# Kernel optimization log

Hardware: AMD Instinct MI355X
Metric: run time of the kernel (lower is better)

## Reference

```python
import jax, jax.numpy as jnp
import numpy as np

M0, M1, H = 128, 64, 8            # scalar mul, vector mul, num heads
AH0, AH1 = 16, 8                  # per-head irreps: 16x0e + 8x1e
D = M0 + 3 * M1                   # 320 node feature dim
DTP0 = M0 + M1                    # 192 scalar channels out of depthwise TP
DTP1 = M0 + 2 * M1                # 256 vector channels out of depthwise TP
WNUM = 2 * M0 + 3 * M1            # 448 TP path weights (uvu, edge mul=1)
RAD_IN, RAD_HID = 32, 64
N_NODES, N_EDGES = 10000, 160000
INV_SQRT3 = 1.0 / np.sqrt(3.0)    # CG norm for 1e x 1e -> 0e
INV_SQRT2 = 1.0 / np.sqrt(2.0)    # CG norm for 1e x 1e -> 1e


def _split(x, m0, m1):
    # e3nn layout: [m0 scalars | m1 vectors * 3 components]
    return x[..., :m0], x[..., m0:].reshape(x.shape[:-1] + (m1, 3))


def _silu(x):
    return x * jax.nn.sigmoid(x)


def _smooth_leaky(x, a=0.2):
    # SmoothLeakyReLU from equiformer
    return 0.5 * (1 + a) * x + 0.5 * (1 - a) * x * (2.0 * jax.nn.sigmoid(x) - 1.0)


def _dtp(s, v, e0, e1, w):
    # depthwise (uvu) tensor product of (M0x0e + M1x1e) with edge attr (1x0e + 1x1e)
    # s [E,M0], v [E,M1,3], e0 [E,1], e1 [E,3], w [E,WNUM] or [WNUM] (internal)
    w1, w2, w3, w4, w5 = jnp.split(w, [M0, 2 * M0, 2 * M0 + M1, 2 * M0 + 2 * M1], axis=-1)
    os1 = w1 * s * e0                                                  # 0e x 0e -> 0e
    os2 = w4 * (jnp.einsum('emc,ec->em', v, e1) * INV_SQRT3)           # 1e x 1e -> 0e
    ov1 = (w2 * s)[..., None] * e1[:, None, :]                         # 0e x 1e -> 1e
    ov2 = w3[..., None] * v * e0[..., None]                            # 1e x 0e -> 1e
    ov3 = w5[..., None] * (jnp.cross(v, e1[:, None, :]) * INV_SQRT2)   # 1e x 1e -> 1e
    return jnp.concatenate([os1, os2], -1), jnp.concatenate([ov1, ov2, ov3], -2)


def _forward(node_input, edge_src, edge_dst, edge_attr, edge_scalars,
             Wsrc_s, Wsrc_v, bsrc, Wdst_s, Wdst_v,
             rad_W1, rad_b1, rad_W2, rad_off,
             Wact_s, bact, Wact_v, Walpha, balpha, w_int,
             Wval_s, bval, Wval_v, alpha_dot, Wproj_s, bproj, Wproj_v):
    N = node_input.shape[0]
    E = edge_src.shape[0]
    s, v = _split(node_input, M0, M1)
    # merge_src / merge_dst: per-irrep linear (bias only on scalars of src)
    ms_s = s @ Wsrc_s + bsrc
    ms_v = jnp.einsum('nmc,mk->nkc', v, Wsrc_v)
    md_s = s @ Wdst_s
    md_v = jnp.einsum('nmc,mk->nkc', v, Wdst_v)
    msg_s = ms_s[edge_src] + md_s[edge_dst]          # [E, M0]
    msg_v = ms_v[edge_src] + md_v[edge_dst]          # [E, M1, 3]
    e0, e1 = edge_attr[:, :1], edge_attr[:, 1:4]
    # radial profile MLP -> edge-dependent TP weights
    w = _silu(edge_scalars @ rad_W1 + rad_b1) @ rad_W2 + rad_off       # [E, WNUM]
    ds, dv = _dtp(msg_s, msg_v, e0, e1, w)           # [E, DTP0], [E, DTP1, 3]
    # alpha branch: linear on TP scalars -> heads -> smooth leaky -> dot
    al = _smooth_leaky((ds @ Walpha + balpha).reshape(E, H, AH0))
    logits = jnp.einsum('ehk,hk->eh', al, alpha_dot[0])                # [E, H]
    # value branch: sep_act.lin + gate
    scal = ds @ Wact_s + bact                        # [E, M0+M1] scalars+gates
    gated_v = jnp.einsum('emc,mk->ekc', dv, Wact_v)  # [E, M1, 3]
    val_s = _silu(scal[:, :M0])
    val_v = gated_v * jax.nn.sigmoid(scal[:, M0:])[..., None]
    # sep_value: depthwise TP with internal weights + linear
    vs, vv = _dtp(val_s, val_v, e0, e1, w_int)
    out_s = vs @ Wval_s + bval                       # [E, H*AH0]
    out_v = jnp.einsum('emc,mk->ekc', vv, Wval_v)    # [E, H*AH1, 3]
    value = jnp.concatenate([out_s.reshape(E, H, AH0),
                             out_v.reshape(E, H, AH1 * 3)], axis=2)    # [E, H, 40]
    # softmax over incoming edges per destination node
    mx = jax.lax.stop_gradient(jax.ops.segment_max(logits, edge_dst, num_segments=N))
    mx = jnp.where(jnp.isfinite(mx), mx, 0.0)
    ex = jnp.exp(logits - mx[edge_dst])
    den = jax.ops.segment_sum(ex, edge_dst, num_segments=N)
    alpha = ex / (den[edge_dst] + 1e-16)             # [E, H]
    agg = jax.ops.segment_sum(value * alpha[..., None], edge_dst, num_segments=N)
    # heads2vec + output projection
    node_s = agg[:, :, :AH0].reshape(N, H * AH0)
    node_v = agg[:, :, AH0:].reshape(N, H * AH1, 3)
    po_s = node_s @ Wproj_s + bproj
    po_v = jnp.einsum('nmc,mk->nkc', node_v, Wproj_v)
    return jnp.concatenate([po_s, po_v.reshape(N, M1 * 3)], axis=1)


def _lin(key, fi, fo):
    return jax.random.normal(key, (fi, fo), jnp.float32) / np.sqrt(fi)


def setup_inputs() -> dict:
    ks = iter(jax.random.split(jax.random.key(0), 40))
    inp = {}
    inp['node_input'] = jax.random.normal(next(ks), (N_NODES, D), jnp.float32)
    inp['edge_src'] = jax.random.randint(next(ks), (N_EDGES,), 0, N_NODES)
    inp['edge_dst'] = jax.random.randint(next(ks), (N_EDGES,), 0, N_NODES)
    inp['edge_attr'] = jax.random.normal(next(ks), (N_EDGES, 4), jnp.float32)
    inp['edge_scalars'] = jax.random.normal(next(ks), (N_EDGES, RAD_IN), jnp.float32)
    inp['Wsrc_s'] = _lin(next(ks), M0, M0)
    inp['Wsrc_v'] = _lin(next(ks), M1, M1)
    inp['bsrc'] = 0.1 * jax.random.normal(next(ks), (M0,), jnp.float32)
    inp['Wdst_s'] = _lin(next(ks), M0, M0)
    inp['Wdst_v'] = _lin(next(ks), M1, M1)
    inp['rad_W1'] = _lin(next(ks), RAD_IN, RAD_HID)
    inp['rad_b1'] = 0.1 * jax.random.normal(next(ks), (RAD_HID,), jnp.float32)
    inp['rad_W2'] = _lin(next(ks), RAD_HID, WNUM)
    inp['rad_off'] = 0.1 * jax.random.normal(next(ks), (WNUM,), jnp.float32)
    inp['Wact_s'] = _lin(next(ks), DTP0, M0 + M1)
    inp['bact'] = 0.1 * jax.random.normal(next(ks), (M0 + M1,), jnp.float32)
    inp['Wact_v'] = _lin(next(ks), DTP1, M1)
    inp['Walpha'] = _lin(next(ks), DTP0, H * AH0)
    inp['balpha'] = 0.1 * jax.random.normal(next(ks), (H * AH0,), jnp.float32)
    inp['w_int'] = jax.random.normal(next(ks), (WNUM,), jnp.float32)
    inp['Wval_s'] = _lin(next(ks), DTP0, H * AH0)
    inp['bval'] = 0.1 * jax.random.normal(next(ks), (H * AH0,), jnp.float32)
    inp['Wval_v'] = _lin(next(ks), DTP1, H * AH1)
    inp['alpha_dot'] = jax.random.normal(next(ks), (1, H, AH0), jnp.float32) / np.sqrt(AH0)
    inp['Wproj_s'] = _lin(next(ks), H * AH0, M0)
    inp['bproj'] = 0.1 * jax.random.normal(next(ks), (M0,), jnp.float32)
    inp['Wproj_v'] = _lin(next(ks), H * AH1, M1)
    return inp


def reference(node_input, edge_src, edge_dst, edge_attr, edge_scalars,
              Wsrc_s, Wsrc_v, bsrc, Wdst_s, Wdst_v,
              rad_W1, rad_b1, rad_W2, rad_off,
              Wact_s, bact, Wact_v, Walpha, balpha, w_int,
              Wval_s, bval, Wval_v, alpha_dot, Wproj_s, bproj, Wproj_v):
    return _forward(node_input, edge_src, edge_dst, edge_attr, edge_scalars,
                    Wsrc_s, Wsrc_v, bsrc, Wdst_s, Wdst_v,
                    rad_W1, rad_b1, rad_W2, rad_off,
                    Wact_s, bact, Wact_v, Walpha, balpha, w_int,
                    Wval_s, bval, Wval_v, alpha_dot, Wproj_s, bproj, Wproj_v)
```

## Files before the change

### kernel.cpp

```cpp
#include <hip/hip_runtime.h>

#define NN 10000
#define NE 160000
#define INV_SQRT3f 0.57735026918962576f
#define INV_SQRT2f 0.70710678118654752f
#define VPLU 640000

typedef short bshort8 __attribute__((ext_vector_type(8)));
typedef float floatx4 __attribute__((ext_vector_type(4)));
#define MFMA16(a,b,c) __builtin_amdgcn_mfma_f32_16x16x32_bf16((a),(b),(c),0,0,0)

__device__ __forceinline__ float sigm(float x){ return 1.f/(1.f+__expf(-x)); }
__device__ __forceinline__ float siluf(float x){ return x*sigm(x); }
__device__ __forceinline__ float sleaky(float x){ return 0.6f*x + 0.4f*x*(2.f*sigm(x)-1.f); }
__device__ __forceinline__ unsigned short f2bf(float f){
  return (unsigned short)((__float_as_uint(f) + 0x8000u)>>16);
}
__device__ __forceinline__ float bf2f(unsigned short h){
  return __uint_as_float(((unsigned)h)<<16);
}
__device__ __forceinline__ unsigned cvtpk(float lo, float hi){
  unsigned r;
  asm("v_cvt_pk_bf16_f32 %0, %1, %2" : "=v"(r) : "v"(lo), "v"(hi));
  return r;
}

#define O_W1   0
#define O_W2   2048
#define O_WAS  30720
#define O_WAVT 67584
#define O_WAVB 75776
#define O_WVS  83968
#define O_WVVT 108544
#define O_WVVB 116736
#define O_WALP 124928
#define SWZ_TOTAL 149504

__global__ __launch_bounds__(256) void k_pre_all(
    const float* __restrict__ x,
    const float* __restrict__ Wsrc_s, const float* __restrict__ Wsrc_v,
    const float* __restrict__ bsrc,
    const float* __restrict__ Wdst_s, const float* __restrict__ Wdst_v,
    unsigned short* __restrict__ ms_s, unsigned short* __restrict__ md_s,
    unsigned short* __restrict__ ms_v, unsigned short* __restrict__ md_v,
    const float* __restrict__ W1, const float* __restrict__ W2,
    const float* __restrict__ WAs, const float* __restrict__ WAv,
    const float* __restrict__ WVs, const float* __restrict__ WVv,
    const float* __restrict__ WAl, const float* __restrict__ w_int,
    unsigned short* __restrict__ swz,
    float* __restrict__ num, float* __restrict__ den, int* __restrict__ cnt) {
  __shared__ __align__(16) float s_s[128*8];
  __shared__ __align__(16) float s_v[192*8];
  const int tid = threadIdx.x;
  const int b = blockIdx.x;
  if (b >= 1834) {
    int base = (b-1834)*256 + tid;
    float4 z = {0.f,0.f,0.f,0.f};
    for (int i = base; i < 800000; i += 554496) ((float4*)num)[i] = z;
    if (base < 20000) ((float4*)den)[base] = z;
    if (base < 10000) cnt[base] = 0;
    return;
  }
  if (b >= 1250) {
    int s = (b-1250)*256 + tid;
    if (s >= SWZ_TOTAL) return;
    const float* src; int base, N, KT, rowOff;
    if      (s < 2048)  { base=O_W1;   src=W1;  N=64;  KT=1; rowOff=0; }
    else if (s < 30720) { base=O_W2;   src=W2;  N=448; KT=2; rowOff=0; }
    else if (s < 67584) { base=O_WAS;  src=WAs; N=192; KT=6; rowOff=0; }
    else if (s < 75776) { base=O_WAVT; src=WAv; N=64;  KT=4; rowOff=0; }
    else if (s < 83968) { base=O_WAVB; src=WAv; N=64;  KT=4; rowOff=128; }
    else if (s < 108544){ base=O_WVS;  src=WVs; N=128; KT=6; rowOff=0; }
    else if (s < 116736){ base=O_WVVT; src=WVv; N=64;  KT=4; rowOff=0; }
    else if (s < 124928){ base=O_WVVB; src=WVv; N=64;  KT=4; rowOff=128; }
    else                { base=O_WALP; src=WAl; N=128; KT=6; rowOff=0; }
    int loc = s - base;
    int j = loc & 7, l = (loc>>3)&63, kt = (loc>>9)%KT, nt = loc/(512*KT);
    int row = kt*32 + (l>>4)*8 + j + rowOff;
    int col = nt*16 + (l&15);
    float scl = 1.f;
    if      (base == O_WVS)  scl = (row < 128) ? w_int[row] : w_int[192+row]*INV_SQRT3f;
    else if (base == O_WVVT) scl = w_int[128+row];
    else if (base == O_WVVB) scl = (row < 192) ? w_int[128+row] : w_int[192+row]*INV_SQRT2f;
    swz[s] = f2bf(src[row*N + col] * scl);
    return;
  }
  const int n0 = b*8;
  for (int idx = tid; idx < 8*320; idx += 256) {
    int n = idx/320, d = idx - n*320;
    float val = x[(n0+n)*320 + d];
    if (d < 128) s_s[d*8+n] = val;
    else         s_v[(d-128)*8+n] = val;
  }
  __syncthreads();
  {
    int g = tid>>7, j = tid&127;
    float accs[4], accd[4];
    float bb = bsrc[j];
    #pragma unroll
    for (int i=0;i<4;i++){ accs[i]=bb; accd[i]=0.f; }
    for (int k=0;k<128;k++) {
      float w1 = Wsrc_s[k*128+j], w2 = Wdst_s[k*128+j];
      float4 sv = *(const float4*)&s_s[k*8+g*4];
      accs[0]+=sv.x*w1; accs[1]+=sv.y*w1; accs[2]+=sv.z*w1; accs[3]+=sv.w*w1;
      accd[0]+=sv.x*w2; accd[1]+=sv.y*w2; accd[2]+=sv.z*w2; accd[3]+=sv.w*w2;
    }
    #pragma unroll
    for (int i=0;i<4;i++){ int n=n0+g*4+i; ms_s[n*128+j]=f2bf(accs[i]); md_s[n*128+j]=f2bf(accd[i]); }
  }
  if (tid < 192) {
    int c = tid>>6, k = tid&63;
    float accs[8], accd[8];
    #pragma unroll
    for (int e=0;e<8;e++){ accs[e]=0.f; accd[e]=0.f; }
    for (int m=0;m<64;m++) {
      float w1 = Wsrc_v[m*64+k], w2 = Wdst_v[m*64+k];
      float4 v0 = *(const float4*)&s_v[(m*3+c)*8];
      float4 v1 = *(const float4*)&s_v[(m*3+c)*8+4];
      accs[0]+=v0.x*w1; accs[1]+=v0.y*w1; accs[2]+=v0.z*w1; accs[3]+=v0.w*w1;
      accs[4]+=v1.x*w1; accs[5]+=v1.y*w1; accs[6]+=v1.z*w1; accs[7]+=v1.w*w1;
      accd[0]+=v0.x*w2; accd[1]+=v0.y*w2; accd[2]+=v0.z*w2; accd[3]+=v0.w*w2;
      accd[4]+=v1.x*w2; accd[5]+=v1.y*w2; accd[6]+=v1.z*w2; accd[7]+=v1.w*w2;
    }
    #pragma unroll
    for (int e=0;e<8;e++){
      int n=n0+e;
      ms_v[c*VPLU + n*64 + k] = f2bf(accs[e]);
      md_v[c*VPLU + n*64 + k] = f2bf(accd[e]);
    }
  }
}

__global__ __launch_bounds__(256) void k_hist(const int* __restrict__ edst,
                                              int* __restrict__ cnt) {
  int e = blockIdx.x*256 + threadIdx.x;
  if (e < NE) atomicAdd(&cnt[edst[e]], 1);
}

__global__ __launch_bounds__(256) void k_scan(const int* __restrict__ cnt,
                                              int* __restrict__ offs) {
  __shared__ int wsum[4];
  const int tid = threadIdx.x;
  const int lane = tid & 63, wave = tid >> 6;
  int v[40]; int s = 0;
  #pragma unroll
  for (int j=0;j<40;j++){ int i = tid*40+j; v[j] = (i<NN)?cnt[i]:0; s += v[j]; }
  int incl = s;
  #pragma unroll
  for (int d=1; d<64; d<<=1) { int t = __shfl_up(incl, d, 64); if (lane>=d) incl += t; }
  if (lane==63) wsum[wave] = incl;
  __syncthreads();
  int wbase = 0;
  for (int w=0; w<wave; ++w) wbase += wsum[w];
  int excl = wbase + incl - s;
  #pragma unroll
  for (int j=0;j<40;j++){ int i = tid*40+j; if (i<NN) offs[i] = excl; excl += v[j]; }
}

__global__ __launch_bounds__(256) void k_scatter(const int* __restrict__ edst,
                                                 int* __restrict__ offs,
                                                 int* __restrict__ perm) {
  int e = blockIdx.x*256 + threadIdx.x;
  if (e < NE) {
    int pos = atomicAdd(&offs[edst[e]], 1);
    perm[pos] = e;
  }
}

__global__ __launch_bounds__(256, 6) void e_all(
    const unsigned short* __restrict__ ms_s, const unsigned short* __restrict__ md_s,
    const unsigned short* __restrict__ ms_v, const unsigned short* __restrict__ md_v,
    const int* __restrict__ esrc, const int* __restrict__ edst,
    const int* __restrict__ perm,
    const float* __restrict__ eattr, const float* __restrict__ escal,
    const float* __restrict__ rad_b1, const float* __restrict__ rad_off,
    const float* __restrict__ bact,
    const float* __restrict__ bval,
    const float* __restrict__ balpha, const float* __restrict__ alpha_dot,
    const unsigned short* __restrict__ swz,
    float* __restrict__ den, float* __restrict__ num) {
  __shared__ __align__(16) char smem[24768];
  unsigned short* ads  = (unsigned short*)smem;
  unsigned short* at1  = (unsigned short*)(smem+6400);
  unsigned short* advb = (unsigned short*)(smem+10752);
  unsigned short* aes  = (unsigned short*)(smem+10752);
  unsigned short* ah   = (unsigned short*)(smem+12032);
  float* vout          = (float*)(smem+10752);
  float* s_e0 = (float*)(smem+23808);
  float* s_e1 = (float*)(smem+23872);
  float* s_ex = (float*)(smem+24064);
  int* s_eid  = (int*)(smem+24576);
  int* s_src  = (int*)(smem+24640);
  int* s_dst  = (int*)(smem+24704);
  const int tid  = threadIdx.x;
  const int lane = tid & 63, wave = tid >> 6;
  const int quad = lane >> 4, l15 = lane & 15;
  const int bswz = (blockIdx.x & 7)*1250 + (blockIdx.x >> 3);
  const int eb = bswz*16;

  if (tid < 16) {
    int eid = perm[eb+tid];
    s_eid[tid] = eid; s_src[tid] = esrc[eid]; s_dst[tid] = edst[eid];
  }
  __syncthreads();
  if (tid >= 64 && tid < 128) {
    int t = tid-64, e = t>>2, q = t&3;
    float a = eattr[s_eid[e]*4+q];
    if (q == 0) s_e0[e] = a; else s_e1[(q-1)*16+e] = a;
  }
  {
    int e = tid>>4, i0 = (tid&15)*2;
    float2 es = *(const float2*)&escal[s_eid[e]*32+i0];
    *(unsigned*)&aes[e*40+i0] = cvtpk(es.x, es.y);
  }
  __syncthreads();

  {
    int nt = wave, col = nt*16 + l15;
    bshort8 a = *(const bshort8*)&aes[l15*40 + quad*8];
    bshort8 b = *(const bshort8*)&swz[O_W1 + (nt*64 + lane)*8];
    float bb = rad_b1[col];
    floatx4 acc = {bb,bb,bb,bb};
    acc = MFMA16(a, b, acc);
    #pragma unroll
    for (int r=0;r<4;r++) ah[(quad*4+r)*72 + col] = f2bf(siluf(acc[r]));
  }
  __syncthreads();

  {
    bshort8 ha0 = *(const bshort8*)&ah[l15*72 + quad*8];
    bshort8 ha1 = *(const bshort8*)&ah[l15*72 + 32 + quad*8];
    __syncthreads();
    int src_[4], dst_[4];
    #pragma unroll
    for (int r=0;r<4;r++){ int e=quad*4+r; src_[r]=s_src[e]; dst_[r]=s_dst[e]; }
    #pragma unroll
    for (int p=0;p<2;p++) {
      int nt1 = wave*2+p, nt2 = nt1+8;
      int m = nt1*16 + l15;
      float o1 = rad_off[m], o2 = rad_off[128+m];
      floatx4 a1 = {o1,o1,o1,o1}, a2 = {o2,o2,o2,o2};
      a1 = MFMA16(ha0, *(const bshort8*)&swz[O_W2 + ((nt1*2+0)*64+lane)*8], a1);
      a1 = MFMA16(ha1, *(const bshort8*)&swz[O_W2 + ((nt1*2+1)*64+lane)*8], a1);
      a2 = MFMA16(ha0, *(const bshort8*)&swz[O_W2 + ((nt2*2+0)*64+lane)*8], a2);
      a2 = MFMA16(ha1, *(const bshort8*)&swz[O_W2 + ((nt2*2+1)*64+lane)*8], a2);
      #pragma unroll
      for (int r=0;r<4;r++) {
        int e = quad*4+r;
        float msgs = bf2f(ms_s[src_[r]*128+m]) + bf2f(md_s[dst_[r]*128+m]);
        ads[e*200+m] = f2bf(a1[r]*msgs*s_e0[e]);
        at1[e*136+m] = f2bf(a2[r]*msgs);
      }
    }
    floatx4 aw3, aw4, aw5;
    {
      int nt = 16 + wave; float o = rad_off[nt*16+l15];
      floatx4 acc = {o,o,o,o};
      acc = MFMA16(ha0, *(const bshort8*)&swz[O_W2 + ((nt*2+0)*64+lane)*8], acc);
      acc = MFMA16(ha1, *(const bshort8*)&swz[O_W2 + ((nt*2+1)*64+lane)*8], acc);
      aw3 = acc;
    }
    {
      int nt = 20 + wave; float o = rad_off[nt*16+l15];
      floatx4 acc = {o,o,o,o};
      acc = MFMA16(ha0, *(const bshort8*)&swz[O_W2 + ((nt*2+0)*64+lane)*8], acc);
      acc = MFMA16(ha1, *(const bshort8*)&swz[O_W2 + ((nt*2+1)*64+lane)*8], acc);
      aw4 = acc;
    }
    {
      int nt = 24 + wave; float o = rad_off[nt*16+l15];
      floatx4 acc = {o,o,o,o};
      acc = MFMA16(ha0, *(const bshort8*)&swz[O_W2 + ((nt*2+0)*64+lane)*8], acc);
      acc = MFMA16(ha1, *(const bshort8*)&swz[O_W2 + ((nt*2+1)*64+lane)*8], acc);
      aw5 = acc;
    }
    const int k = wave*16 + l15;
    #pragma unroll
    for (int r=0;r<4;r++) {
      int e = quad*4 + r;
      int sb = src_[r]*64 + k, db = dst_[r]*64 + k;
      float vx = bf2f(ms_v[0*VPLU+sb]) + bf2f(md_v[0*VPLU+db]);
      float vy = bf2f(ms_v[1*VPLU+sb]) + bf2f(md_v[1*VPLU+db]);
      float vz = bf2f(ms_v[2*VPLU+sb]) + bf2f(md_v[2*VPLU+db]);
      float ex1 = s_e1[0+e], ey1 = s_e1[16+e], ez1 = s_e1[32+e];
      float e0 = s_e0[e];
      float d = vx*ex1 + vy*ey1 + vz*ez1;
      ads[e*200+128+k] = f2bf(aw4[r]*d*INV_SQRT3f);
      float w3v = aw3[r]*e0;
      float w5  = aw5[r]*INV_SQRT2f;
      advb[0*2176 + e*136 + k] = f2bf(w3v*vx);
      advb[1*2176 + e*136 + k] = f2bf(w3v*vy);
      advb[2*2176 + e*136 + k] = f2bf(w3v*vz);
      advb[0*2176 + e*136 + 64+k] = f2bf(w5*(vy*ez1 - vz*ey1));
      advb[1*2176 + e*136 + 64+k] = f2bf(w5*(vz*ex1 - vx*ez1));
      advb[2*2176 + e*136 + 64+k] = f2bf(w5*(vx*ey1 - vy*ex1));
    }
  }
  __syncthreads();

  floatx4 sc0, sc1, sc2, gsa, gb0, gb1, gb2;
  {
    bshort8 fa[6];
    #pragma unroll
    for (int kt=0;kt<6;kt++) fa[kt] = *(const bshort8*)&ads[l15*200 + kt*32 + quad*8];
    #pragma unroll
    for (int t=0;t<2;t++) {
      int h = wave*2 + t;
      int col = h*16 + l15;
      float bb = balpha[col];
      floatx4 acc = {bb,bb,bb,bb};
      #pragma unroll
      for (int kt=0;kt<6;kt++)
        acc = MFMA16(fa[kt], *(const bshort8*)&swz[O_WALP + ((h*6+kt)*64+lane)*8], acc);
      float ad = alpha_dot[col];
      float exv[4];
      #pragma unroll
      for (int r=0;r<4;r++) {
        float p = sleaky(acc[r])*ad;
        p += __shfl_xor(p, 1);
        p += __shfl_xor(p, 2);
        p += __shfl_xor(p, 4);
        p += __shfl_xor(p, 8);
        float ex = __expf(p);
        exv[r] = ex;
        if (l15 == 0) s_ex[(quad*4+r)*8+h] = ex;
      }
      if (l15 == 0) {
        float racc = exv[0]; int cur = s_dst[quad*4];
        #pragma unroll
        for (int r=1;r<4;r++) {
          int d = s_dst[quad*4+r];
          if (d != cur) { atomicAdd(&den[cur*8+h], racc); racc = 0.f; cur = d; }
          racc += exv[r];
        }
        atomicAdd(&den[cur*8+h], racc);
      }
    }
    {
      float bb = bact[wave*16 + l15];
      floatx4 a0 = {bb,bb,bb,bb};
      #pragma unroll
      for (int kt=0;kt<6;kt++)
        a0 = MFMA16(fa[kt], *(const bshort8*)&swz[O_WAS + ((wave*6+kt)*64+lane)*8], a0);
      sc0 = a0;
    }
    {
      float bb = bact[(wave+4)*16 + l15];
      floatx4 a1 = {bb,bb,bb,bb};
      #pragma unroll
      for (int kt=0;kt<6;kt++)
        a1 = MFMA16(fa[kt], *(const bshort8*)&swz[O_WAS + (((wave+4)*6+kt)*64+lane)*8], a1);
      sc1 = a1;
    }
    {
      float bb = bact[(wave+8)*16 + l15];
      floatx4 a2 = {bb,bb,bb,bb};
      #pragma unroll
      for (int kt=0;kt<6;kt++)
        a2 = MFMA16(fa[kt], *(const bshort8*)&swz[O_WAS + (((wave+8)*6+kt)*64+lane)*8], a2);
      sc2 = a2;
    }
    bshort8 ft[4];
    #pragma unroll
    for (int kt=0;kt<4;kt++) ft[kt] = *(const bshort8*)&at1[l15*136 + kt*32 + quad*8];
    {
      floatx4 acc = {0.f,0.f,0.f,0.f};
      #pragma unroll
      for (int kt=0;kt<4;kt++)
        acc = MFMA16(ft[kt], *(const bshort8*)&swz[O_WAVT + ((wave*4+kt)*64+lane)*8], acc);
      gsa = acc;
    }
    #pragma unroll
    for (int c=0;c<3;c++) {
      floatx4 acc = {0.f,0.f,0.f,0.f};
      #pragma unroll
      for (int kt=0;kt<4;kt++) {
        bshort8 fb = *(const bshort8*)&advb[c*2176 + l15*136 + kt*32 + quad*8];
        acc = MFMA16(fb, *(const bshort8*)&swz[O_WAVB + ((wave*4+kt)*64+lane)*8], acc);
      }
      if (c==0) gb0 = acc; else if (c==1) gb1 = acc; else gb2 = acc;
    }
  }
  __syncthreads();

  {
    const int k = wave*16 + l15;
    #pragma unroll
    for (int r=0;r<4;r++) {
      int row = quad*4 + r;
      float e0 = s_e0[row];
      {
        float v = siluf(sc0[r]);
        ads[row*200+k] = f2bf(v*e0);
        at1[row*136+k] = f2bf(v);
      }
      {
        float v = siluf(sc1[r]);
        ads[row*200+64+k] = f2bf(v*e0);
        at1[row*136+64+k] = f2bf(v);
      }
      {
        float sg = sigm(sc2[r]);
        float gs = gsa[r];
        float ex1 = s_e1[0+row], ey1 = s_e1[16+row], ez1 = s_e1[32+row];
        float v0 = (gs*ex1 + gb0[r])*sg;
        float v1 = (gs*ey1 + gb1[r])*sg;
        float v2 = (gs*ez1 + gb2[r])*sg;
        float d = v0*ex1 + v1*ey1 + v2*ez1;
        ads[row*200+128+k] = f2bf(d);
        advb[0*2176 + row*136 + k] = f2bf(v0*e0);
        advb[1*2176 + row*136 + k] = f2bf(v1*e0);
        advb[2*2176 + row*136 + k] = f2bf(v2*e0);
        advb[0*2176 + row*136 + 64+k] = f2bf(v1*ez1 - v2*ey1);
        advb[1*2176 + row*136 + 64+k] = f2bf(v2*ex1 - v0*ez1);
        advb[2*2176 + row*136 + 64+k] = f2bf(v0*ey1 - v1*ex1);
      }
    }
  }
  __syncthreads();

  {
    bshort8 ft[4];
    #pragma unroll
    for (int kt=0;kt<4;kt++) ft[kt] = *(const bshort8*)&at1[l15*136 + kt*32 + quad*8];
    floatx4 vsh = {0.f,0.f,0.f,0.f};
    #pragma unroll
    for (int kt=0;kt<4;kt++)
      vsh = MFMA16(ft[kt], *(const bshort8*)&swz[O_WVVT + ((wave*4+kt)*64+lane)*8], vsh);
    floatx4 vb0, vb1, vb2;
    #pragma unroll
    for (int c=0;c<3;c++) {
      floatx4 acc = {0.f,0.f,0.f,0.f};
      #pragma unroll
      for (int kt=0;kt<4;kt++) {
        bshort8 fb = *(const bshort8*)&advb[c*2176 + l15*136 + kt*32 + quad*8];
        acc = MFMA16(fb, *(const bshort8*)&swz[O_WVVB + ((wave*4+kt)*64+lane)*8], acc);
      }
      if (c==0) vb0 = acc; else if (c==1) vb1 = acc; else vb2 = acc;
    }
    __syncthreads();
    const int k = wave*16 + l15;
    const int h = k>>3, q = k&7;
    #pragma unroll
    for (int r=0;r<4;r++) {
      int row = quad*4 + r;
      float exr = s_ex[row*8+h];
      vout[row*194 + h*24 + q*3 + 0] = (vb0[r] + s_e1[0*16+row]*vsh[r])*exr;
      vout[row*194 + h*24 + q*3 + 1] = (vb1[r] + s_e1[1*16+row]*vsh[r])*exr;
      vout[row*194 + h*24 + q*3 + 2] = (vb2[r] + s_e1[2*16+row]*vsh[r])*exr;
    }
  }
  __syncthreads();

  if (tid < 192) {
    const int jj = tid;
    const int h = jj/24, rr = jj - h*24;
    float acc = 0.f; int cur = s_dst[0];
    #pragma unroll
    for (int e = 0; e < 16; ++e) {
      int d = s_dst[e];
      if (d != cur) { atomicAdd(&num[cur*320 + h*40 + 16 + rr], acc); acc = 0.f; cur = d; }
      acc += vout[e*194 + jj];
    }
    atomicAdd(&num[cur*320 + h*40 + 16 + rr], acc);
  }
  __syncthreads();

  {
    bshort8 fa[6];
    #pragma unroll
    for (int kt=0;kt<6;kt++) fa[kt] = *(const bshort8*)&ads[l15*200 + kt*32 + quad*8];
    #pragma unroll
    for (int t=0;t<2;t++) {
      int h = wave + 4*t;
      float bb = bval[h*16 + l15];
      floatx4 acc = {bb,bb,bb,bb};
      #pragma unroll
      for (int kt=0;kt<6;kt++)
        acc = MFMA16(fa[kt], *(const bshort8*)&swz[O_WVS + ((h*6+kt)*64+lane)*8], acc);
      #pragma unroll
      for (int r=0;r<4;r++) {
        int row = quad*4 + r;
        vout[row*132 + h*16 + l15] = acc[r]*s_ex[row*8+h];
      }
    }
  }
  __syncthreads();

  if (tid < 128) {
    const int j = tid, h = j>>4, jj = j&15;
    float acc = 0.f; int cur = s_dst[0];
    #pragma unroll
    for (int e = 0; e < 16; ++e) {
      int d = s_dst[e];
      if (d != cur) { atomicAdd(&num[cur*320 + h*40 + jj], acc); acc = 0.f; cur = d; }
      acc += vout[e*132 + j];
    }
    atomicAdd(&num[cur*320 + h*40 + jj], acc);
  }
}

__global__ __launch_bounds__(256) void node_post(
    const float* __restrict__ num, const float* __restrict__ den,
    const float* __restrict__ Wproj_s, const float* __restrict__ bproj,
    const float* __restrict__ Wproj_v, float* __restrict__ out) {
  __shared__ __align__(16) float s_ns[128*8];
  __shared__ __align__(16) float s_nv[192*8];
  const int tid = threadIdx.x;
  const int n0 = blockIdx.x*8;
  for (int idx = tid; idx < 8*320; idx += 256) {
    int n = idx/320, j = idx - n*320;
    int h = j/40, r = j - h*40;
    float a = num[(n0+n)*320+j] / (den[(n0+n)*8+h] + 1e-16f);
    if (r < 16) s_ns[(h*16+r)*8+n] = a;
    else        s_nv[(h*24 + (r-16))*8+n] = a;
  }
  __syncthreads();
  {
    int g = tid>>7, j = tid&127;
    float acc[4]; float b = bproj[j];
    #pragma unroll
    for (int i=0;i<4;i++) acc[i]=b;
    for (int k=0;k<128;k++) {
      float wv = Wproj_s[k*128+j];
      float4 s4 = *(const float4*)&s_ns[k*8+g*4];
      acc[0]+=s4.x*wv; acc[1]+=s4.y*wv; acc[2]+=s4.z*wv; acc[3]+=s4.w*wv;
    }
    #pragma unroll
    for (int i=0;i<4;i++) out[(n0+g*4+i)*320 + j] = acc[i];
  }
  if (tid < 192) {
    int c = tid>>6, k = tid&63;
    float acc[8];
    #pragma unroll
    for (int e=0;e<8;e++) acc[e]=0.f;
    for (int m=0;m<64;m++) {
      float wv = Wproj_v[m*64+k];
      float4 v0 = *(const float4*)&s_nv[(m*3+c)*8];
      float4 v1 = *(const float4*)&s_nv[(m*3+c)*8+4];
      acc[0]+=v0.x*wv; acc[1]+=v0.y*wv; acc[2]+=v0.z*wv; acc[3]+=v0.w*wv;
      acc[4]+=v1.x*wv; acc[5]+=v1.y*wv; acc[6]+=v1.z*wv; acc[7]+=v1.w*wv;
    }
    #pragma unroll
    for (int e=0;e<8;e++) out[(n0+e)*320 + 128 + k*3 + c] = acc[e];
  }
}

extern "C" void kernel_launch(void* const* d_in, const int* in_sizes, int n_in,
                              void* d_out, int out_size, void* d_ws, size_t ws_size,
                              hipStream_t stream) {
  (void)in_sizes; (void)n_in; (void)out_size; (void)ws_size;
  const float* node_input = (const float*)d_in[0];
  const int*   esrc       = (const int*)d_in[1];
  const int*   edst       = (const int*)d_in[2];
  const float* eattr      = (const float*)d_in[3];
  const float* escal      = (const float*)d_in[4];
  const float* Wsrc_s     = (const float*)d_in[5];
  const float* Wsrc_v     = (const float*)d_in[6];
  const float* bsrc       = (const float*)d_in[7];
  const float* Wdst_s     = (const float*)d_in[8];
  const float* Wdst_v     = (const float*)d_in[9];
  const float* rad_W1     = (const float*)d_in[10];
  const float* rad_b1     = (const float*)d_in[11];
  const float* rad_W2     = (const float*)d_in[12];
  const float* rad_off    = (const float*)d_in[13];
  const float* Wact_s     = (const float*)d_in[14];
  const float* bact       = (const float*)d_in[15];
  const float* Wact_v     = (const float*)d_in[16];
  const float* Walpha     = (const float*)d_in[17];
  const float* balpha     = (const float*)d_in[18];
  const float* w_int      = (const float*)d_in[19];
  const float* Wval_s     = (const float*)d_in[20];
  const float* bval       = (const float*)d_in[21];
  const float* Wval_v     = (const float*)d_in[22];
  const float* alpha_dot  = (const float*)d_in[23];
  const float* Wproj_s    = (const float*)d_in[24];
  const float* bproj      = (const float*)d_in[25];
  const float* Wproj_v    = (const float*)d_in[26];
  float* out = (float*)d_out;

  char* wsb = (char*)d_ws;
  unsigned short* ms_s16 = (unsigned short*)(wsb);
  unsigned short* md_s16 = (unsigned short*)(wsb + 2560000);
  unsigned short* ms_v16 = (unsigned short*)(wsb + 5120000);
  unsigned short* md_v16 = (unsigned short*)(wsb + 8960000);
  float* den             = (float*)(wsb + 12800000);
  float* num             = (float*)(wsb + 13120000);
  unsigned short* swz    = (unsigned short*)(wsb + 25920000);
  int* cnt  = (int*)(wsb + 26220032);
  int* offs = (int*)(wsb + 26260032);
  int* perm = (int*)(wsb + 26300032);

  k_pre_all<<<4000, 256, 0, stream>>>(node_input, Wsrc_s, Wsrc_v, bsrc, Wdst_s, Wdst_v,
                                      ms_s16, md_s16, ms_v16, md_v16,
                                      rad_W1, rad_W2, Wact_s, Wact_v, Wval_s, Wval_v,
                                      Walpha, w_int, swz, num, den, cnt);
  k_hist<<<625, 256, 0, stream>>>(edst, cnt);
  k_scan<<<1, 256, 0, stream>>>(cnt, offs);
  k_scatter<<<625, 256, 0, stream>>>(edst, offs, perm);
  e_all<<<10000, 256, 0, stream>>>(ms_s16, md_s16, ms_v16, md_v16, esrc, edst, perm, eattr, escal,
                                   rad_b1, rad_off, bact, bval,
                                   balpha, alpha_dot, swz, den, num);
  node_post<<<1250, 256, 0, stream>>>(num, den, Wproj_s, bproj, Wproj_v, out);
}
```

Baseline: 383.4 us.

## Interleave vector xyz into padded 4-wide layout and widen node tiles

```diff
diff --git a/kernel.cpp b/kernel.cpp
--- a/kernel.cpp
+++ b/kernel.cpp
@@ -4,7 +4,6 @@
 #define NE 160000
 #define INV_SQRT3f 0.57735026918962576f
 #define INV_SQRT2f 0.70710678118654752f
-#define VPLU 640000
 
 typedef short bshort8 __attribute__((ext_vector_type(8)));
 typedef float floatx4 __attribute__((ext_vector_type(4)));
@@ -24,6 +23,8 @@
   asm("v_cvt_pk_bf16_f32 %0, %1, %2" : "=v"(r) : "v"(lo), "v"(hi));
   return r;
 }
+__device__ __forceinline__ float lo16f(unsigned u){ return __uint_as_float(u<<16); }
+__device__ __forceinline__ float hi16f(unsigned u){ return __uint_as_float(u & 0xffff0000u); }
 
 #define O_W1   0
 #define O_W2   2048
@@ -49,20 +50,20 @@
     const float* __restrict__ WAl, const float* __restrict__ w_int,
     unsigned short* __restrict__ swz,
     float* __restrict__ num, float* __restrict__ den, int* __restrict__ cnt) {
-  __shared__ __align__(16) float s_s[128*8];
-  __shared__ __align__(16) float s_v[192*8];
+  __shared__ __align__(16) float s_s[128*16];
+  __shared__ __align__(16) float s_v[192*16];
   const int tid = threadIdx.x;
   const int b = blockIdx.x;
-  if (b >= 1834) {
-    int base = (b-1834)*256 + tid;
+  if (b >= 1209) {
+    int base = (b-1209)*256 + tid;
     float4 z = {0.f,0.f,0.f,0.f};
     for (int i = base; i < 800000; i += 554496) ((float4*)num)[i] = z;
     if (base < 20000) ((float4*)den)[base] = z;
     if (base < 10000) cnt[base] = 0;
     return;
   }
-  if (b >= 1250) {
-    int s = (b-1250)*256 + tid;
+  if (b >= 625) {
+    int s = (b-625)*256 + tid;
     if (s >= SWZ_TOTAL) return;
     const float* src; int base, N, KT, rowOff;
     if      (s < 2048)  { base=O_W1;   src=W1;  N=64;  KT=1; rowOff=0; }
@@ -85,48 +86,54 @@
     swz[s] = f2bf(src[row*N + col] * scl);
     return;
   }
-  const int n0 = b*8;
-  for (int idx = tid; idx < 8*320; idx += 256) {
+  const int n0 = b*16;
+  for (int idx = tid; idx < 16*320; idx += 256) {
     int n = idx/320, d = idx - n*320;
     float val = x[(n0+n)*320 + d];
-    if (d < 128) s_s[d*8+n] = val;
-    else         s_v[(d-128)*8+n] = val;
+    if (d < 128) s_s[d*16+n] = val;
+    else         s_v[(d-128)*16+n] = val;
   }
   __syncthreads();
   {
     int g = tid>>7, j = tid&127;
-    float accs[4], accd[4];
+    float accs[8], accd[8];
     float bb = bsrc[j];
     #pragma unroll
-    for (int i=0;i<4;i++){ accs[i]=bb; accd[i]=0.f; }
+    for (int i=0;i<8;i++){ accs[i]=bb; accd[i]=0.f; }
     for (int k=0;k<128;k++) {
       float w1 = Wsrc_s[k*128+j], w2 = Wdst_s[k*128+j];
-      float4 sv = *(const float4*)&s_s[k*8+g*4];
-      accs[0]+=sv.x*w1; accs[1]+=sv.y*w1; accs[2]+=sv.z*w1; accs[3]+=sv.w*w1;
-      accd[0]+=sv.x*w2; accd[1]+=sv.y*w2; accd[2]+=sv.z*w2; accd[3]+=sv.w*w2;
-    }
-    #pragma unroll
-    for (int i=0;i<4;i++){ int n=n0+g*4+i; ms_s[n*128+j]=f2bf(accs[i]); md_s[n*128+j]=f2bf(accd[i]); }
+      float4 a0 = *(const float4*)&s_s[k*16+g*8];
+      float4 a1 = *(const float4*)&s_s[k*16+g*8+4];
+      accs[0]+=a0.x*w1; accs[1]+=a0.y*w1; accs[2]+=a0.z*w1; accs[3]+=a0.w*w1;
+      accs[4]+=a1.x*w1; accs[5]+=a1.y*w1; accs[6]+=a1.z*w1; accs[7]+=a1.w*w1;
+      accd[0]+=a0.x*w2; accd[1]+=a0.y*w2; accd[2]+=a0.z*w2; accd[3]+=a0.w*w2;
+      accd[4]+=a1.x*w2; accd[5]+=a1.y*w2; accd[6]+=a1.z*w2; accd[7]+=a1.w*w2;
+    }
+    #pragma unroll
+    for (int i=0;i<8;i++){ int n=n0+g*8+i; ms_s[n*128+j]=f2bf(accs[i]); md_s[n*128+j]=f2bf(accd[i]); }
   }
   if (tid < 192) {
     int c = tid>>6, k = tid&63;
-    float accs[8], accd[8];
-    #pragma unroll
-    for (int e=0;e<8;e++){ accs[e]=0.f; accd[e]=0.f; }
-    for (int m=0;m<64;m++) {
-      float w1 = Wsrc_v[m*64+k], w2 = Wdst_v[m*64+k];
-      float4 v0 = *(const float4*)&s_v[(m*3+c)*8];
-      float4 v1 = *(const float4*)&s_v[(m*3+c)*8+4];
-      accs[0]+=v0.x*w1; accs[1]+=v0.y*w1; accs[2]+=v0.z*w1; accs[3]+=v0.w*w1;
-      accs[4]+=v1.x*w1; accs[5]+=v1.y*w1; accs[6]+=v1.z*w1; accs[7]+=v1.w*w1;
-      accd[0]+=v0.x*w2; accd[1]+=v0.y*w2; accd[2]+=v0.z*w2; accd[3]+=v0.w*w2;
-      accd[4]+=v1.x*w2; accd[5]+=v1.y*w2; accd[6]+=v1.z*w2; accd[7]+=v1.w*w2;
-    }
-    #pragma unroll
-    for (int e=0;e<8;e++){
-      int n=n0+e;
-      ms_v[c*VPLU + n*64 + k] = f2bf(accs[e]);
-      md_v[c*VPLU + n*64 + k] = f2bf(accd[e]);
+    #pragma unroll
+    for (int half=0; half<2; ++half) {
+      float accs[8], accd[8];
+      #pragma unroll
+      for (int e=0;e<8;e++){ accs[e]=0.f; accd[e]=0.f; }
+      for (int m=0;m<64;m++) {
+        float w1 = Wsrc_v[m*64+k], w2 = Wdst_v[m*64+k];
+        float4 v0 = *(const float4*)&s_v[(m*3+c)*16 + half*8];
+        float4 v1 = *(const float4*)&s_v[(m*3+c)*16 + half*8 + 4];
+        accs[0]+=v0.x*w1; accs[1]+=v0.y*w1; accs[2]+=v0.z*w1; accs[3]+=v0.w*w1;
+        accs[4]+=v1.x*w1; accs[5]+=v1.y*w1; accs[6]+=v1.z*w1; accs[7]+=v1.w*w1;
+        accd[0]+=v0.x*w2; accd[1]+=v0.y*w2; accd[2]+=v0.z*w2; accd[3]+=v0.w*w2;
+        accd[4]+=v1.x*w2; accd[5]+=v1.y*w2; accd[6]+=v1.z*w2; accd[7]+=v1.w*w2;
+      }
+      #pragma unroll
+      for (int e=0;e<8;e++){
+        int n = n0 + half*8 + e;
+        ms_v[(n*64+k)*4 + c] = f2bf(accs[e]);
+        md_v[(n*64+k)*4 + c] = f2bf(accd[e]);
+      }
     }
   }
 }
@@ -139,12 +146,15 @@
 
 __global__ __launch_bounds__(256) void k_scan(const int* __restrict__ cnt,
                                               int* __restrict__ offs) {
+  __shared__ int sc[10240];
   __shared__ int wsum[4];
   const int tid = threadIdx.x;
   const int lane = tid & 63, wave = tid >> 6;
+  for (int i = tid; i < 10240; i += 256) sc[i] = (i < NN) ? cnt[i] : 0;
+  __syncthreads();
   int v[40]; int s = 0;
   #pragma unroll
-  for (int j=0;j<40;j++){ int i = tid*40+j; v[j] = (i<NN)?cnt[i]:0; s += v[j]; }
+  for (int j=0;j<40;j++){ v[j] = sc[tid*40+j]; s += v[j]; }
   int incl = s;
   #pragma unroll
   for (int d=1; d<64; d<<=1) { int t = __shfl_up(incl, d, 64); if (lane>=d) incl += t; }
@@ -278,10 +288,11 @@
     #pragma unroll
     for (int r=0;r<4;r++) {
       int e = quad*4 + r;
-      int sb = src_[r]*64 + k, db = dst_[r]*64 + k;
-      float vx = bf2f(ms_v[0*VPLU+sb]) + bf2f(md_v[0*VPLU+db]);
-      float vy = bf2f(ms_v[1*VPLU+sb]) + bf2f(md_v[1*VPLU+db]);
-      float vz = bf2f(ms_v[2*VPLU+sb]) + bf2f(md_v[2*VPLU+db]);
+      uint2 us = *(const uint2*)&ms_v[(src_[r]*64 + k)*4];
+      uint2 ud = *(const uint2*)&md_v[(dst_[r]*64 + k)*4];
+      float vx = lo16f(us.x) + lo16f(ud.x);
+      float vy = hi16f(us.x) + hi16f(ud.x);
+      float vz = lo16f(us.y) + lo16f(ud.y);
       float ex1 = s_e1[0+e], ey1 = s_e1[16+e], ez1 = s_e1[32+e];
       float e0 = s_e0[e];
       float d = vx*ex1 + vy*ey1 + vz*ez1;
@@ -370,15 +381,20 @@
         acc = MFMA16(ft[kt], *(const bshort8*)&swz[O_WAVT + ((wave*4+kt)*64+lane)*8], acc);
       gsa = acc;
     }
-    #pragma unroll
-    for (int c=0;c<3;c++) {
-      floatx4 acc = {0.f,0.f,0.f,0.f};
-      #pragma unroll
-      for (int kt=0;kt<4;kt++) {
-        bshort8 fb = *(const bshort8*)&advb[c*2176 + l15*136 + kt*32 + quad*8];
-        acc = MFMA16(fb, *(const bshort8*)&swz[O_WAVB + ((wave*4+kt)*64+lane)*8], acc);
-      }
-      if (c==0) gb0 = acc; else if (c==1) gb1 = acc; else gb2 = acc;
+    {
+      bshort8 wb[4];
+      #pragma unroll
+      for (int kt=0;kt<4;kt++) wb[kt] = *(const bshort8*)&swz[O_WAVB + ((wave*4+kt)*64+lane)*8];
+      #pragma unroll
+      for (int c=0;c<3;c++) {
+        floatx4 acc = {0.f,0.f,0.f,0.f};
+        #pragma unroll
+        for (int kt=0;kt<4;kt++) {
+          bshort8 fb = *(const bshort8*)&advb[c*2176 + l15*136 + kt*32 + quad*8];
+          acc = MFMA16(fb, wb[kt], acc);
+        }
+        if (c==0) gb0 = acc; else if (c==1) gb1 = acc; else gb2 = acc;
+      }
     }
   }
   __syncthreads();
@@ -428,15 +444,20 @@
     for (int kt=0;kt<4;kt++)
       vsh = MFMA16(ft[kt], *(const bshort8*)&swz[O_WVVT + ((wave*4+kt)*64+lane)*8], vsh);
     floatx4 vb0, vb1, vb2;
-    #pragma unroll
-    for (int c=0;c<3;c++) {
-      floatx4 acc = {0.f,0.f,0.f,0.f};
-      #pragma unroll
-      for (int kt=0;kt<4;kt++) {
-        bshort8 fb = *(const bshort8*)&advb[c*2176 + l15*136 + kt*32 + quad*8];
-        acc = MFMA16(fb, *(const bshort8*)&swz[O_WVVB + ((wave*4+kt)*64+lane)*8], acc);
-      }
-      if (c==0) vb0 = acc; else if (c==1) vb1 = acc; else vb2 = acc;
+    {
+      bshort8 wb[4];
+      #pragma unroll
+      for (int kt=0;kt<4;kt++) wb[kt] = *(const bshort8*)&swz[O_WVVB + ((wave*4+kt)*64+lane)*8];
+      #pragma unroll
+      for (int c=0;c<3;c++) {
+        floatx4 acc = {0.f,0.f,0.f,0.f};
+        #pragma unroll
+        for (int kt=0;kt<4;kt++) {
+          bshort8 fb = *(const bshort8*)&advb[c*2176 + l15*136 + kt*32 + quad*8];
+          acc = MFMA16(fb, wb[kt], acc);
+        }
+        if (c==0) vb0 = acc; else if (c==1) vb1 = acc; else vb2 = acc;
+      }
     }
     __syncthreads();
     const int k = wave*16 + l15;
@@ -504,45 +525,50 @@
     const float* __restrict__ num, const float* __restrict__ den,
     const float* __restrict__ Wproj_s, const float* __restrict__ bproj,
     const float* __restrict__ Wproj_v, float* __restrict__ out) {
-  __shared__ __align__(16) float s_ns[128*8];
-  __shared__ __align__(16) float s_nv[192*8];
+  __shared__ __align__(16) float s_ns[128*16];
+  __shared__ __align__(16) float s_nv[192*16];
   const int tid = threadIdx.x;
-  const int n0 = blockIdx.x*8;
-  for (int idx = tid; idx < 8*320; idx += 256) {
+  const int n0 = blockIdx.x*16;
+  for (int idx = tid; idx < 16*320; idx += 256) {
     int n = idx/320, j = idx - n*320;
     int h = j/40, r = j - h*40;
     float a = num[(n0+n)*320+j] / (den[(n0+n)*8+h] + 1e-16f);
-    if (r < 16) s_ns[(h*16+r)*8+n] = a;
-    else        s_nv[(h*24 + (r-16))*8+n] = a;
+    if (r < 16) s_ns[(h*16+r)*16+n] = a;
+    else        s_nv[(h*24 + (r-16))*16+n] = a;
   }
   __syncthreads();
   {
     int g = tid>>7, j = tid&127;
-    float acc[4]; float b = bproj[j];
-    #pragma unroll
-    for (int i=0;i<4;i++) acc[i]=b;
+    float acc[8]; float b = bproj[j];
+    #pragma unroll
+    for (int i=0;i<8;i++) acc[i]=b;
     for (int k=0;k<128;k++) {
       float wv = Wproj_s[k*128+j];
-      float4 s4 = *(const float4*)&s_ns[k*8+g*4];
-      acc[0]+=s4.x*wv; acc[1]+=s4.y*wv; acc[2]+=s4.z*wv; acc[3]+=s4.w*wv;
-    }
-    #pragma unroll
-    for (int i=0;i<4;i++) out[(n0+g*4+i)*320 + j] = acc[i];
+      float4 a0 = *(const float4*)&s_ns[k*16+g*8];
+      float4 a1 = *(const float4*)&s_ns[k*16+g*8+4];
+      acc[0]+=a0.x*wv; acc[1]+=a0.y*wv; acc[2]+=a0.z*wv; acc[3]+=a0.w*wv;
+      acc[4]+=a1.x*wv; acc[5]+=a1.y*wv; acc[6]+=a1.z*wv; acc[7]+=a1.w*wv;
+    }
+    #pragma unroll
+    for (int i=0;i<8;i++) out[(n0+g*8+i)*320 + j] = acc[i];
   }
   if (tid < 192) {
     int c = tid>>6, k = tid&63;
-    float acc[8];
-    #pragma unroll
-    for (int e=0;e<8;e++) acc[e]=0.f;
-    for (int m=0;m<64;m++) {
-      float wv = Wproj_v[m*64+k];
-      float4 v0 = *(const float4*)&s_nv[(m*3+c)*8];
-      float4 v1 = *(const float4*)&s_nv[(m*3+c)*8+4];
-      acc[0]+=v0.x*wv; acc[1]+=v0.y*wv; acc[2]+=v0.z*wv; acc[3]+=v0.w*wv;
-      acc[4]+=v1.x*wv; acc[5]+=v1.y*wv; acc[6]+=v1.z*wv; acc[7]+=v1.w*wv;
-    }
-    #pragma unroll
-    for (int e=0;e<8;e++) out[(n0+e)*320 + 128 + k*3 + c] = acc[e];
+    #pragma unroll
+    for (int half=0; half<2; ++half) {
+      float acc[8];
+      #pragma unroll
+      for (int e=0;e<8;e++) acc[e]=0.f;
+      for (int m=0;m<64;m++) {
+        float wv = Wproj_v[m*64+k];
+        float4 v0 = *(const float4*)&s_nv[(m*3+c)*16 + half*8];
+        float4 v1 = *(const float4*)&s_nv[(m*3+c)*16 + half*8 + 4];
+        acc[0]+=v0.x*wv; acc[1]+=v0.y*wv; acc[2]+=v0.z*wv; acc[3]+=v0.w*wv;
+        acc[4]+=v1.x*wv; acc[5]+=v1.y*wv; acc[6]+=v1.z*wv; acc[7]+=v1.w*wv;
+      }
+      #pragma unroll
+      for (int e=0;e<8;e++) out[(n0+half*8+e)*320 + 128 + k*3 + c] = acc[e];
+    }
   }
 }
 
@@ -582,24 +608,24 @@
   char* wsb = (char*)d_ws;
   unsigned short* ms_s16 = (unsigned short*)(wsb);
   unsigned short* md_s16 = (unsigned short*)(wsb + 2560000);
-  unsigned short* ms_v16 = (unsigned short*)(wsb + 5120000);
-  unsigned short* md_v16 = (unsigned short*)(wsb + 8960000);
-  float* den             = (float*)(wsb + 12800000);
-  float* num             = (float*)(wsb + 13120000);
-  unsigned short* swz    = (unsigned short*)(wsb + 25920000);
-  int* cnt  = (int*)(wsb + 26220032);
-  int* offs = (int*)(wsb + 26260032);
-  int* perm = (int*)(wsb + 26300032);
-
-  k_pre_all<<<4000, 256, 0, stream>>>(node_input, Wsrc_s, Wsrc_v, bsrc, Wdst_s, Wdst_v,
-                                      ms_s16, md_s16, ms_v16, md_v16,
+  unsigned short* ms_v4  = (unsigned short*)(wsb + 5120000);
+  unsigned short* md_v4  = (unsigned short*)(wsb + 10240000);
+  float* den             = (float*)(wsb + 15360000);
+  float* num             = (float*)(wsb + 15680000);
+  unsigned short* swz    = (unsigned short*)(wsb + 28480000);
+  int* cnt  = (int*)(wsb + 28779008);
+  int* offs = (int*)(wsb + 28819008);
+  int* perm = (int*)(wsb + 28859008);
+
+  k_pre_all<<<3375, 256, 0, stream>>>(node_input, Wsrc_s, Wsrc_v, bsrc, Wdst_s, Wdst_v,
+                                      ms_s16, md_s16, ms_v4, md_v4,
                                       rad_W1, rad_W2, Wact_s, Wact_v, Wval_s, Wval_v,
                                       Walpha, w_int, swz, num, den, cnt);
   k_hist<<<625, 256, 0, stream>>>(edst, cnt);
   k_scan<<<1, 256, 0, stream>>>(cnt, offs);
   k_scatter<<<625, 256, 0, stream>>>(edst, offs, perm);
-  e_all<<<10000, 256, 0, stream>>>(ms_s16, md_s16, ms_v16, md_v16, esrc, edst, perm, eattr, escal,
+  e_all<<<10000, 256, 0, stream>>>(ms_s16, md_s16, ms_v4, md_v4, esrc, edst, perm, eattr, escal,
                                    rad_b1, rad_off, bact, bval,
                                    balpha, alpha_dot, swz, den, num);
-  node_post<<<1250, 256, 0, stream>>>(num, den, Wproj_s, bproj, Wproj_v, out);
-}
+  node_post<<<625, 256, 0, stream>>>(num, den, Wproj_s, bproj, Wproj_v, out);
+}
```

Measured after the change: 441.0 us. +15.0%, slower.
